# Kernel tuning notes

Measured on AMD Instinct MI355X. Metric: run time of the kernel, lower is better.

## Reference

```python
import jax, jax.numpy as jnp
import numpy as np

B, S, H, C = 512, 16, 501, 7


def _uniform(k, shape, scale):
    return jax.random.uniform(k, shape, minval=-scale, maxval=scale, dtype=jnp.float32)


def setup_inputs() -> dict:
    key = jax.random.key(0)
    ks = jax.random.split(key, 20)
    s = 1.0 / np.sqrt(H)        # torch default init bound for Linear(H, .) and GRUCell
    se = 1.0 / np.sqrt(2 * H)   # Linear(2H, 1)
    z = jax.random.normal(ks[0], (B, H), jnp.float32)
    # strictly-lower-triangular 0/1 adjacency (DAG, ancestors have smaller index)
    dep = jax.random.randint(ks[1], (B, S, S), 0, 2).astype(jnp.float32)
    dep_graph = dep * jnp.tril(jnp.ones((S, S), jnp.float32), k=-1)
    node_encoding = jax.nn.one_hot(jax.random.randint(ks[2], (B, S), 0, C), C, dtype=jnp.float32)
    return {
        "z": z,
        "dep_graph": dep_graph,
        "node_encoding": node_encoding,
        "W_lin1": _uniform(ks[3], (H, H), s), "b_lin1": _uniform(ks[4], (H,), s),
        "W_vert": _uniform(ks[5], (C, H), s), "b_vert": _uniform(ks[6], (C,), s),
        "W_edge": _uniform(ks[7], (1, 2 * H), se), "b_edge": _uniform(ks[8], (1,), se),
        "W_gate": _uniform(ks[9], (H, H), s), "b_gate": _uniform(ks[10], (H,), s),
        "W_map": _uniform(ks[11], (H, H), s), "b_map": _uniform(ks[12], (H,), s),
        "W_ih": _uniform(ks[13], (3 * H, C), s), "b_ih": _uniform(ks[14], (3 * H,), s),
        "W_hh": _uniform(ks[15], (3 * H, H), s), "b_hh": _uniform(ks[16], (3 * H,), s),
    }


def _forward(z, dep_graph, node_encoding, W_lin1, b_lin1, W_vert, b_vert, W_edge, b_edge,
             W_gate, b_gate, W_map, b_map, W_ih, b_ih, W_hh, b_hh):
    Bs, Ss, _ = dep_graph.shape
    Hs = W_lin1.shape[0]

    def gru(x, h):  # torch.nn.GRUCell math
        gi = x @ W_ih.T + b_ih
        gh = h @ W_hh.T + b_hh
        i_r, i_z, i_n = jnp.split(gi, 3, axis=-1)
        h_r, h_z, h_n = jnp.split(gh, 3, axis=-1)
        r = jax.nn.sigmoid(i_r + h_r)
        u = jax.nn.sigmoid(i_z + h_z)
        n = jnp.tanh(i_n + r * h_n)
        return (1.0 - u) * n + u * h

    col = jnp.arange(Ss)

    def outer_step(carry, idx):
        graph_state, nhs = carry  # nhs: (B, S, H) node_hidden_state
        logits = jax.nn.softmax(graph_state @ W_vert.T + b_vert, axis=-1)  # add_vertex
        x_idx = jax.lax.dynamic_index_in_dim(node_encoding, idx, axis=1, keepdims=False)  # (B, C)
        row0 = jax.lax.dynamic_index_in_dim(dep_graph, idx, axis=1, keepdims=False)       # (B, S)

        def inner_step(ic, t):  # v_j = idx-1, ..., 0 (masked when v_j < 0)
            hv, nhs_i, row, edges = ic
            v_j = idx - 1 - t
            active = v_j >= 0
            vj = jnp.maximum(v_j, 0)
            hidden_j = jax.lax.dynamic_index_in_dim(nhs_i, vj, axis=1, keepdims=False)  # (B, H)
            p = jax.nn.sigmoid(jnp.concatenate([hv, hidden_j], axis=-1) @ W_edge.T + b_edge)  # (B,1)
            is_edge = (p[:, 0] >= 0.5).astype(z.dtype)  # hard threshold, as in source
            # emulates the in-place `ancestors[:, :v_j] = 0` on the dep_graph row
            row_new = jnp.where(col[None, :] < vj, 0.0, row)
            anc = (nhs_i * row_new[:, :, None]).reshape(-1, Hs)  # (B*S, H)
            h_in = (jax.nn.sigmoid(anc @ W_gate.T + b_gate) * (anc @ W_map.T + b_map)
                    ).reshape(Bs, Ss, Hs).sum(axis=1)  # gated-sum message aggregation
            hv_new = gru(x_idx, h_in)
            nhs_new = jax.lax.dynamic_update_index_in_dim(nhs_i, hv_new, idx, axis=1)
            edges = jnp.where(active, edges.at[:, vj].set(is_edge), edges)
            hv = jnp.where(active, hv_new, hv)
            nhs_i = jnp.where(active, nhs_new, nhs_i)
            row = jnp.where(active, row_new, row)
            return (hv, nhs_i, row, edges), None

        edges0 = jnp.zeros((Bs, Ss), z.dtype)
        (hv, nhs2, _, edges), _ = jax.lax.scan(
            inner_step, (graph_state, nhs, row0, edges0), jnp.arange(Ss - 1))
        # index == 0: no ancestors; hv = GRU(x_0, graph_state) (source leaves hv undefined here)
        hv = jnp.where(idx == 0, gru(x_idx, graph_state), hv)
        nhs3 = jax.lax.dynamic_update_index_in_dim(nhs2, hv, idx, axis=1)
        return (hv, nhs3), (logits, edges)

    graph_state0 = z @ W_lin1.T + b_lin1
    nhs0 = jnp.zeros((Bs, Ss, Hs), z.dtype)
    _, (enc, rows) = jax.lax.scan(outer_step, (graph_state0, nhs0), jnp.arange(Ss))
    gen_dep_graph = jnp.transpose(rows, (1, 0, 2))      # (B, S, S)
    gen_node_encoding = jnp.transpose(enc, (1, 0, 2))   # (B, S, C)
    return gen_dep_graph, gen_node_encoding


def reference(z, dep_graph, node_encoding, W_lin1, b_lin1, W_vert, b_vert, W_edge, b_edge,
              W_gate, b_gate, W_map, b_map, W_ih, b_ih, W_hh, b_hh):
    return _forward(z, dep_graph, node_encoding, W_lin1, b_lin1, W_vert, b_vert, W_edge,
                    b_edge, W_gate, b_gate, W_map, b_map, W_ih, b_ih, W_hh, b_hh)
```

## Files before the change

kernel.cpp:

```cpp
#include <hip/hip_runtime.h>
#include <math.h>

#define BB 512
#define SS 16
#define HH 501
#define CC 7
#define CH 128
#define PBK (4*BB)
#define OFF_ENC (BB*SS*SS)

#define BUFSZ (132*PBK)
#define O_BUFIN 0
#define O_BUFH  BUFSZ
#define O_ALIST (2*BUFSZ)
#define O_ELIST (O_ALIST + SS*BB)
#define O_CLS   (O_ELIST + SS*BB)

__device__ __forceinline__ float4 ld4(const float* p) { return *(const float4*)p; }
__device__ __forceinline__ float sigm(float x) { return 1.f / (1.f + expf(-x)); }

__device__ __forceinline__ int PACK(int k, int b) {
    return (k >> 2) * PBK + b * 4 + (k & 3);
}

__global__ __launch_bounds__(256) void k_prep(
    const float* __restrict__ z, const float* __restrict__ xenc,
    float* __restrict__ bufH, int* __restrict__ cls, float* __restrict__ out)
{
    const int b = blockIdx.x, tid = threadIdx.x;
    if (b < 256) {
        __shared__ float t[32][33];
        const int bt = b >> 4, kt = b & 15;
        const int b0 = bt * 32, k0 = kt * 32;
        const int tx = tid & 31, ty = tid >> 5;
#pragma unroll
        for (int i = 0; i < 4; ++i) {
            int row = ty + i * 8;
            t[row][tx] = (k0 + tx < HH) ? z[(b0 + row) * HH + k0 + tx] : 0.f;
        }
        __syncthreads();
#pragma unroll
        for (int i = 0; i < 4; ++i) {
            int row = ty + i * 8;
            int k = k0 + row;
            float v = (k < HH) ? t[tx][row] : 0.f;
            bufH[PACK(k, b0 + tx)] = v;
        }
    } else if (b < 264) {
        int base = (b - 256) * 1024 + tid * 4;
#pragma unroll
        for (int q = 0; q < 4; ++q) {
            int e = base + q; int s = e >> 9, bb = e & 511;
            const float* xp = xenc + (bb * SS + s) * CC;
            int c = 0;
#pragma unroll
            for (int cc = 0; cc < CC; ++cc) if (xp[cc] > 0.5f) c = cc;
            cls[s * BB + bb] = c;
        }
    } else {
        float4 z4 = make_float4(0.f, 0.f, 0.f, 0.f);
        float4* o4 = (float4*)out;
#pragma unroll
        for (int q = 0; q < 4; ++q)
            o4[(b - 264) * 1024 + q * 256 + tid] = z4;
    }
}

__global__ __launch_bounds__(256) void k_g0(
    const float* __restrict__ act, const float* __restrict__ W,
    const float* __restrict__ blin1, float* __restrict__ dst)
{
    __shared__ float wl[4][520];
    const int tid = threadIdx.x, lane = tid & 63;
    const int wv = __builtin_amdgcn_readfirstlane(tid >> 6);
    const int rg = blockIdx.x >> 2, ch = blockIdx.x & 3;
    const int r = rg * 4 + wv;
#pragma unroll
    for (int j = 0; j < 4; ++j) {
        int rr = rg * 4 + j;
        const float* src = W + (size_t)min(rr, HH - 1) * HH;
        bool ok = rr < HH;
        for (int k = tid; k < 512; k += 256)
            wl[j][k] = (ok && k < HH) ? src[k] : 0.f;
    }
    __syncthreads();
    const int c0 = ch * 128 + lane, c1 = c0 + 64;
    const float* a0 = act + c0 * 4;
    const float* a1 = act + c1 * 4;
    float4 A0[4], A1[4], Wb[2];
#pragma unroll
    for (int q = 0; q < 3; ++q) { A0[q] = ld4(a0 + q * PBK); A1[q] = ld4(a1 + q * PBK); }
    Wb[0] = ld4(&wl[wv][0]);
    float s0 = 0.f, s1 = 0.f;
#pragma unroll 4
    for (int kc = 0; kc < CH; ++kc) {
        int kn = kc + 3;
        A0[kn & 3] = ld4(a0 + (size_t)kn * PBK);
        A1[kn & 3] = ld4(a1 + (size_t)kn * PBK);
        int kw = min(kc + 1, CH - 1);
        Wb[(kc + 1) & 1] = ld4(&wl[wv][kw * 4]);
        float4 w = Wb[kc & 1], x0 = A0[kc & 3], x1 = A1[kc & 3];
        s0 = fmaf(w.x, x0.x, s0); s0 = fmaf(w.y, x0.y, s0);
        s0 = fmaf(w.z, x0.z, s0); s0 = fmaf(w.w, x0.w, s0);
        s1 = fmaf(w.x, x1.x, s1); s1 = fmaf(w.y, x1.y, s1);
        s1 = fmaf(w.z, x1.z, s1); s1 = fmaf(w.w, x1.w, s1);
    }
    if (r < HH) {
        float bv = blin1[r];
        dst[PACK(r, c0)] = s0 + bv;
        dst[PACK(r, c1)] = s1 + bv;
    }
}

__global__ __launch_bounds__(256) void k_gru(
    const float* __restrict__ act, const float* __restrict__ Whh,
    const int* __restrict__ cls,
    const float* __restrict__ bhh, const float* __restrict__ Wih,
    const float* __restrict__ bih, int idx, float* __restrict__ dst)
{
    __shared__ float wl[12][520];
    const int tid = threadIdx.x, lane = tid & 63;
    const int wv = __builtin_amdgcn_readfirstlane(tid >> 6);
    const int rg = blockIdx.x >> 2, ch = blockIdx.x & 3;
    const int r = rg * 4 + wv;
#pragma unroll
    for (int j = 0; j < 12; ++j) {
        int g = j >> 2, rl = j & 3, rr = rg * 4 + rl;
        const float* src = Whh + (size_t)(g * HH + min(rr, HH - 1)) * HH;
        bool ok = rr < HH;
        for (int k = tid; k < 512; k += 256)
            wl[j][k] = (ok && k < HH) ? src[k] : 0.f;
    }
    const int c0 = ch * 128 + lane, c1 = c0 + 64;
    const int cc0 = cls[idx * BB + c0], cc1 = cls[idx * BB + c1];
    const float hp0 = act[PACK(min(r, HH - 1), c0)];
    const float hp1 = act[PACK(min(r, HH - 1), c1)];
    __syncthreads();
    const float* a0 = act + c0 * 4;
    const float* a1 = act + c1 * 4;
    float4 A0[4], A1[4], Wb[2][3];
#pragma unroll
    for (int q = 0; q < 3; ++q) { A0[q] = ld4(a0 + q * PBK); A1[q] = ld4(a1 + q * PBK); }
#pragma unroll
    for (int g = 0; g < 3; ++g) Wb[0][g] = ld4(&wl[g * 4 + wv][0]);
    float acc[6] = {};
#pragma unroll 4
    for (int kc = 0; kc < CH; ++kc) {
        int kn = kc + 3;
        A0[kn & 3] = ld4(a0 + (size_t)kn * PBK);
        A1[kn & 3] = ld4(a1 + (size_t)kn * PBK);
        int kw = min(kc + 1, CH - 1);
#pragma unroll
        for (int g = 0; g < 3; ++g) Wb[(kc + 1) & 1][g] = ld4(&wl[g * 4 + wv][kw * 4]);
        float4 x0 = A0[kc & 3], x1 = A1[kc & 3];
#pragma unroll
        for (int g = 0; g < 3; ++g) {
            float4 w = Wb[kc & 1][g];
            acc[g*2+0] = fmaf(w.x, x0.x, acc[g*2+0]); acc[g*2+0] = fmaf(w.y, x0.y, acc[g*2+0]);
            acc[g*2+0] = fmaf(w.z, x0.z, acc[g*2+0]); acc[g*2+0] = fmaf(w.w, x0.w, acc[g*2+0]);
            acc[g*2+1] = fmaf(w.x, x1.x, acc[g*2+1]); acc[g*2+1] = fmaf(w.y, x1.y, acc[g*2+1]);
            acc[g*2+1] = fmaf(w.z, x1.z, acc[g*2+1]); acc[g*2+1] = fmaf(w.w, x1.w, acc[g*2+1]);
        }
    }
    if (r < HH) {
        float bi0 = bih[r], bi1 = bih[HH + r], bi2 = bih[2 * HH + r];
        float bh0 = bhh[r], bh1 = bhh[HH + r], bh2 = bhh[2 * HH + r];
        float w0c0 = Wih[(0 * HH + r) * CC + cc0], w1c0 = Wih[(1 * HH + r) * CC + cc0],
              w2c0 = Wih[(2 * HH + r) * CC + cc0];
        float w0c1 = Wih[(0 * HH + r) * CC + cc1], w1c1 = Wih[(1 * HH + r) * CC + cc1],
              w2c1 = Wih[(2 * HH + r) * CC + cc1];
        {
            float rgt = sigm(w0c0 + bi0 + acc[0] + bh0);
            float ugt = sigm(w1c0 + bi1 + acc[2] + bh1);
            float ngt = tanhf(w2c0 + bi2 + rgt * (acc[4] + bh2));
            dst[PACK(r, c0)] = (1.f - ugt) * ngt + ugt * hp0;
        }
        {
            float rgt = sigm(w0c1 + bi0 + acc[1] + bh0);
            float ugt = sigm(w1c1 + bi1 + acc[3] + bh1);
            float ngt = tanhf(w2c1 + bi2 + rgt * (acc[5] + bh2));
            dst[PACK(r, c1)] = (1.f - ugt) * ngt + ugt * hp1;
        }
    }
}

__global__ __launch_bounds__(256) void k_post(
    const float* __restrict__ actH, const float* __restrict__ actIn,
    const float* __restrict__ Wgate, const float* __restrict__ bgate,
    const float* __restrict__ Wmap,  const float* __restrict__ bmap,
    const float* __restrict__ dep,
    const float* __restrict__ Wedge, const float* __restrict__ bedge,
    const float* __restrict__ Wvert, const float* __restrict__ bvert,
    int idx, int ngemm, int dsrc,
    float* __restrict__ dst, float* __restrict__ Alist,
    float* __restrict__ Elist, float* __restrict__ out)
{
    __shared__ float wl[9][520];
    const int tid = threadIdx.x, lane = tid & 63;
    const int wv = __builtin_amdgcn_readfirstlane(tid >> 6);
    if ((int)blockIdx.x < ngemm) {
        const int rg = blockIdx.x >> 2, ch = blockIdx.x & 3;
        const int r = rg * 4 + wv;
#pragma unroll
        for (int j = 0; j < 8; ++j) {
            int t2 = j >> 2, rl = j & 3, rr = rg * 4 + rl;
            const float* src = (t2 ? Wmap : Wgate) + (size_t)min(rr, HH - 1) * HH;
            bool ok = rr < HH;
            for (int k = tid; k < 512; k += 256)
                wl[j][k] = (ok && k < HH) ? src[k] : 0.f;
        }
        const int c0 = ch * 128 + lane, c1 = c0 + 64;
        const float d0 = dep[c0 * (SS * SS) + (idx + 1) * SS + idx];
        const float d1 = dep[c1 * (SS * SS) + (idx + 1) * SS + idx];
        __syncthreads();
        const float* a0 = actH + c0 * 4;
        const float* a1 = actH + c1 * 4;
        float4 A0[4], A1[4], Wb[2][2];
#pragma unroll
        for (int q = 0; q < 3; ++q) { A0[q] = ld4(a0 + q * PBK); A1[q] = ld4(a1 + q * PBK); }
#pragma unroll
        for (int t2 = 0; t2 < 2; ++t2) Wb[0][t2] = ld4(&wl[t2 * 4 + wv][0]);
        float acc[4] = {};
#pragma unroll 4
        for (int kc = 0; kc < CH; ++kc) {
            int kn = kc + 3;
            A0[kn & 3] = ld4(a0 + (size_t)kn * PBK);
            A1[kn & 3] = ld4(a1 + (size_t)kn * PBK);
            int kw = min(kc + 1, CH - 1);
#pragma unroll
            for (int t2 = 0; t2 < 2; ++t2) Wb[(kc + 1) & 1][t2] = ld4(&wl[t2 * 4 + wv][kw * 4]);
            float4 x0 = A0[kc & 3], x1 = A1[kc & 3];
#pragma unroll
            for (int t2 = 0; t2 < 2; ++t2) {
                float4 w = Wb[kc & 1][t2];
                acc[t2*2+0] = fmaf(w.x, x0.x, acc[t2*2+0]); acc[t2*2+0] = fmaf(w.y, x0.y, acc[t2*2+0]);
                acc[t2*2+0] = fmaf(w.z, x0.z, acc[t2*2+0]); acc[t2*2+0] = fmaf(w.w, x0.w, acc[t2*2+0]);
                acc[t2*2+1] = fmaf(w.x, x1.x, acc[t2*2+1]); acc[t2*2+1] = fmaf(w.y, x1.y, acc[t2*2+1]);
                acc[t2*2+1] = fmaf(w.z, x1.z, acc[t2*2+1]); acc[t2*2+1] = fmaf(w.w, x1.w, acc[t2*2+1]);
            }
        }
        if (r < HH) {
            float bgv = bgate[r], bmv = bmap[r];
            float c0v = sigm(bgv) * bmv;
            float f0 = sigm(acc[0] + bgv) * (acc[2] + bmv);
            float f1 = sigm(acc[1] + bgv) * (acc[3] + bmv);
            dst[PACK(r, c0)] = (d0 != 0.f) ? (f0 + 15.f * c0v) : (16.f * c0v);
            dst[PACK(r, c1)] = (d1 != 0.f) ? (f1 + 15.f * c0v) : (16.f * c0v);
        }
    } else {
#pragma unroll
        for (int j = 0; j < 9; ++j) {
            const float* src = (j < 2) ? (Wedge + j * HH) : (Wvert + (j - 2) * HH);
            for (int k = tid; k < 512; k += 256)
                wl[j][k] = (k < HH) ? src[k] : 0.f;
        }
        __syncthreads();
        const int db = ((int)blockIdx.x - ngemm) * 256 + tid;
        const float* hp = (dsrc ? actH : actIn) + db * 4;
        float4 Ab[4];
#pragma unroll
        for (int q = 0; q < 3; ++q) Ab[q] = ld4(hp + q * PBK);
        float p[9];
#pragma unroll
        for (int j = 0; j < 9; ++j) p[j] = 0.f;
#pragma unroll 4
        for (int kc = 0; kc < CH; ++kc) {
            int kn = kc + 3;
            Ab[kn & 3] = ld4(hp + (size_t)kn * PBK);
            float4 x = Ab[kc & 3];
#pragma unroll
            for (int j = 0; j < 9; ++j) {
                float4 w = ld4(&wl[j][kc * 4]);
                p[j] = fmaf(w.x, x.x, p[j]); p[j] = fmaf(w.y, x.y, p[j]);
                p[j] = fmaf(w.z, x.z, p[j]); p[j] = fmaf(w.w, x.w, p[j]);
            }
        }
        if (idx >= 0) { Alist[idx * BB + db] = p[0]; Elist[idx * BB + db] = p[1]; }
        if (idx <= SS - 2) {
            float lv[CC]; float mx = -1e30f;
#pragma unroll
            for (int c = 0; c < CC; ++c) { lv[c] = p[2 + c] + bvert[c]; mx = fmaxf(mx, lv[c]); }
            float sum = 0.f; float ev[CC];
#pragma unroll
            for (int c = 0; c < CC; ++c) { ev[c] = expf(lv[c] - mx); sum += ev[c]; }
            float inv = 1.f / sum;
#pragma unroll
            for (int c = 0; c < CC; ++c)
                out[OFF_ENC + (db * SS + (idx + 1)) * CC + c] = ev[c] * inv;
        }
        if (idx >= 1) {
            float be = bedge[0];
            float aprev = Alist[(idx - 1) * BB + db], eprev = Elist[(idx - 1) * BB + db];
            out[db * SS * SS + idx * SS + (idx - 1)] =
                (aprev + eprev + be >= 0.f) ? 1.f : 0.f;
            for (int vj = 0; vj <= idx - 2; ++vj)
                out[db * SS * SS + idx * SS + vj] =
                    (p[0] + Elist[vj * BB + db] + be >= 0.f) ? 1.f : 0.f;
        }
    }
}

extern "C" void kernel_launch(void* const* d_in, const int* in_sizes, int n_in,
                              void* d_out, int out_size, void* d_ws, size_t ws_size,
                              hipStream_t stream)
{
    const float* z     = (const float*)d_in[0];
    const float* dep   = (const float*)d_in[1];
    const float* xenc  = (const float*)d_in[2];
    const float* Wlin1 = (const float*)d_in[3];
    const float* blin1 = (const float*)d_in[4];
    const float* Wvert = (const float*)d_in[5];
    const float* bvert = (const float*)d_in[6];
    const float* Wedge = (const float*)d_in[7];
    const float* bedge = (const float*)d_in[8];
    const float* Wgate = (const float*)d_in[9];
    const float* bgate = (const float*)d_in[10];
    const float* Wmap  = (const float*)d_in[11];
    const float* bmap  = (const float*)d_in[12];
    const float* Wih   = (const float*)d_in[13];
    const float* bih   = (const float*)d_in[14];
    const float* Whh   = (const float*)d_in[15];
    const float* bhh   = (const float*)d_in[16];
    float* out = (float*)d_out;

    float* ws    = (float*)d_ws;
    float* bufIn = ws + O_BUFIN;
    float* bufH  = ws + O_BUFH;
    float* Alist = ws + O_ALIST;
    float* Elist = ws + O_ELIST;
    int*   cls   = (int*)(ws + O_CLS);

    k_prep<<<296, 256, 0, stream>>>(z, xenc, bufH, cls, out);
    k_g0<<<504, 256, 0, stream>>>(bufH, Wlin1, blin1, bufIn);
    k_post<<<2, 256, 0, stream>>>(bufH, bufIn, Wgate, bgate, Wmap, bmap, dep,
                                  Wedge, bedge, Wvert, bvert, -1, 0, 0,
                                  bufIn, Alist, Elist, out);
    for (int idx = 0; idx < SS; ++idx) {
        k_gru<<<504, 256, 0, stream>>>(bufIn, Whh, cls, bhh, Wih, bih, idx, bufH);
        int ng = (idx < SS - 1) ? 504 : 0;
        k_post<<<ng + 2, 256, 0, stream>>>(bufH, bufIn, Wgate, bgate, Wmap, bmap,
                                           dep, Wedge, bedge, Wvert, bvert,
                                           idx, ng, 1,
                                           bufIn, Alist, Elist, out);
    }
}
```

Baseline: 1.319 ms.

## Move GRU and post GEMMs to bf16x3 split-precision MFMA with prepacked weights

Replaces the FP32 FMA GEMV-style kernels with MFMA 16x16x32 bf16 matrix-core kernels. FP32 accuracy is approximated by splitting each operand into hi and lo bf16 parts and issuing three MFMAs per product. Weights are converted once into a fragment-ready bf16 layout. Activations are also written in transposed bf16 hi/lo form alongside the packed fp32 buffer. This targets the FP32 ALU cost of the recurrent per-step GEMMs, at the price of extra conversion work, more workspace, and a small precision risk.

```diff
diff --git a/kernel.cpp b/kernel.cpp
--- a/kernel.cpp
+++ b/kernel.cpp
@@ -5,7 +5,7 @@
 #define SS 16
 #define HH 501
 #define CC 7
-#define CH 128
+#define KP 512
 #define PBK (4*BB)
 #define OFF_ENC (BB*SS*SS)
 
@@ -15,288 +15,376 @@
 #define O_ALIST (2*BUFSZ)
 #define O_ELIST (O_ALIST + SS*BB)
 #define O_CLS   (O_ELIST + SS*BB)
-
-__device__ __forceinline__ float4 ld4(const float* p) { return *(const float4*)p; }
+#define O_ZT    (O_CLS + SS*BB)
+#define O_INT   (O_ZT  + 262144)
+#define O_HT    (O_INT + 262144)
+#define O_WLIN  (O_HT  + 262144)
+#define O_WPOST (O_WLIN + 262144)
+#define O_WHH   (O_WPOST + 524288)
+#define O_WDOT  (O_WHH + 786432)
+
+typedef __attribute__((ext_vector_type(8))) short bfrag;
+typedef __attribute__((ext_vector_type(4))) float ffrag;
+
 __device__ __forceinline__ float sigm(float x) { return 1.f / (1.f + expf(-x)); }
 
-__device__ __forceinline__ int PACK(int k, int b) {
-    return (k >> 2) * PBK + b * 4 + (k & 3);
-}
-
-__global__ __launch_bounds__(256) void k_prep(
+__device__ __forceinline__ unsigned short f2bf(float x) {
+    unsigned u = __float_as_uint(x);
+    u = u + 0x7fffu + ((u >> 16) & 1u);
+    return (unsigned short)(u >> 16);
+}
+__device__ __forceinline__ float bf2f(unsigned short h) {
+    return __uint_as_float(((unsigned)h) << 16);
+}
+
+__global__ __launch_bounds__(256) void k_wprep(
+    const float* __restrict__ Wlin1, const float* __restrict__ Wgate,
+    const float* __restrict__ Wmap,  const float* __restrict__ Whh,
+    const float* __restrict__ Wedge, const float* __restrict__ Wvert,
+    unsigned short* __restrict__ wlin, unsigned short* __restrict__ wpost,
+    unsigned short* __restrict__ whhf, unsigned short* __restrict__ wdot)
+{
+    const int id = blockIdx.x * 256 + threadIdx.x;
+    const int slot = id >> 10, rem = id & 1023, s = rem >> 6, lane = rem & 63;
+    const int rloc = lane & 15;
+    const int k0 = s * 32 + ((lane >> 4) << 3);
+    const float* src; unsigned short* dst; int dslot; bool valid;
+    if (slot < 32) {
+        int row = slot * 16 + rloc; valid = row < HH;
+        src = Wlin1 + (size_t)(valid ? row : 0) * HH; dst = wlin; dslot = slot;
+    } else if (slot < 96) {
+        int p = slot - 32, g = p >> 5, mt = p & 31;
+        int row = mt * 16 + rloc; valid = row < HH;
+        src = (g ? Wmap : Wgate) + (size_t)(valid ? row : 0) * HH; dst = wpost; dslot = p;
+    } else if (slot < 192) {
+        int p = slot - 96, g = p >> 5, mt = p & 31;
+        int row = mt * 16 + rloc; valid = row < HH;
+        src = Whh + (size_t)(g * HH + (valid ? row : 0)) * HH; dst = whhf; dslot = p;
+    } else {
+        int row = rloc; dst = wdot; dslot = 0;
+        if (row < 2)      { src = Wedge + (size_t)row * HH; valid = true; }
+        else if (row < 9) { src = Wvert + (size_t)(row - 2) * HH; valid = true; }
+        else              { src = Wedge; valid = false; }
+    }
+    unsigned h[8], l[8];
+#pragma unroll
+    for (int j = 0; j < 8; ++j) {
+        int k = k0 + j;
+        float w = (valid && k < HH) ? src[k] : 0.f;
+        unsigned short hb = f2bf(w);
+        h[j] = hb; l[j] = f2bf(w - bf2f(hb));
+    }
+    size_t base = ((size_t)dslot * 32 + s * 2) * 512 + lane * 8;
+    uint4 uh, ul;
+    uh.x = h[0] | (h[1] << 16); uh.y = h[2] | (h[3] << 16);
+    uh.z = h[4] | (h[5] << 16); uh.w = h[6] | (h[7] << 16);
+    ul.x = l[0] | (l[1] << 16); ul.y = l[2] | (l[3] << 16);
+    ul.z = l[4] | (l[5] << 16); ul.w = l[6] | (l[7] << 16);
+    *(uint4*)&dst[base] = uh;
+    *(uint4*)&dst[base + 512] = ul;
+}
+
+__global__ __launch_bounds__(256) void k_prep2(
     const float* __restrict__ z, const float* __restrict__ xenc,
-    float* __restrict__ bufH, int* __restrict__ cls, float* __restrict__ out)
+    unsigned short* __restrict__ zTh, unsigned short* __restrict__ zTl,
+    int* __restrict__ cls, float* __restrict__ out)
 {
     const int b = blockIdx.x, tid = threadIdx.x;
-    if (b < 256) {
-        __shared__ float t[32][33];
-        const int bt = b >> 4, kt = b & 15;
-        const int b0 = bt * 32, k0 = kt * 32;
-        const int tx = tid & 31, ty = tid >> 5;
-#pragma unroll
-        for (int i = 0; i < 4; ++i) {
-            int row = ty + i * 8;
-            t[row][tx] = (k0 + tx < HH) ? z[(b0 + row) * HH + k0 + tx] : 0.f;
-        }
-        __syncthreads();
-#pragma unroll
-        for (int i = 0; i < 4; ++i) {
-            int row = ty + i * 8;
-            int k = k0 + row;
-            float v = (k < HH) ? t[tx][row] : 0.f;
-            bufH[PACK(k, b0 + tx)] = v;
-        }
-    } else if (b < 264) {
-        int base = (b - 256) * 1024 + tid * 4;
+    if (b < 128) {
+        const int id = b * 256 + tid;
+        const int bb = id >> 6, kc = id & 63, k0 = kc * 8;
+        unsigned h[8], l[8];
+#pragma unroll
+        for (int j = 0; j < 8; ++j) {
+            int k = k0 + j;
+            float w = (k < HH) ? z[(size_t)bb * HH + k] : 0.f;
+            unsigned short hb = f2bf(w);
+            h[j] = hb; l[j] = f2bf(w - bf2f(hb));
+        }
+        uint4 uh, ul;
+        uh.x = h[0] | (h[1] << 16); uh.y = h[2] | (h[3] << 16);
+        uh.z = h[4] | (h[5] << 16); uh.w = h[6] | (h[7] << 16);
+        ul.x = l[0] | (l[1] << 16); ul.y = l[2] | (l[3] << 16);
+        ul.z = l[4] | (l[5] << 16); ul.w = l[6] | (l[7] << 16);
+        *(uint4*)&zTh[(size_t)bb * 512 + k0] = uh;
+        *(uint4*)&zTl[(size_t)bb * 512 + k0] = ul;
+    } else if (b < 136) {
+        int base = (b - 128) * 1024 + tid * 4;
 #pragma unroll
         for (int q = 0; q < 4; ++q) {
-            int e = base + q; int s = e >> 9, bb = e & 511;
-            const float* xp = xenc + (bb * SS + s) * CC;
-            int c = 0;
-#pragma unroll
-            for (int cc = 0; cc < CC; ++cc) if (xp[cc] > 0.5f) c = cc;
-            cls[s * BB + bb] = c;
+            int e = base + q, sI = e >> 9, bb = e & 511;
+            const float* xp = xenc + ((size_t)bb * SS + sI) * CC;
+            int cv = 0;
+#pragma unroll
+            for (int cc = 0; cc < CC; ++cc) if (xp[cc] > 0.5f) cv = cc;
+            cls[sI * BB + bb] = cv;
         }
     } else {
         float4 z4 = make_float4(0.f, 0.f, 0.f, 0.f);
         float4* o4 = (float4*)out;
 #pragma unroll
         for (int q = 0; q < 4; ++q)
-            o4[(b - 264) * 1024 + q * 256 + tid] = z4;
-    }
-}
-
-__global__ __launch_bounds__(256) void k_g0(
-    const float* __restrict__ act, const float* __restrict__ W,
-    const float* __restrict__ blin1, float* __restrict__ dst)
-{
-    __shared__ float wl[4][520];
-    const int tid = threadIdx.x, lane = tid & 63;
-    const int wv = __builtin_amdgcn_readfirstlane(tid >> 6);
-    const int rg = blockIdx.x >> 2, ch = blockIdx.x & 3;
-    const int r = rg * 4 + wv;
-#pragma unroll
-    for (int j = 0; j < 4; ++j) {
-        int rr = rg * 4 + j;
-        const float* src = W + (size_t)min(rr, HH - 1) * HH;
-        bool ok = rr < HH;
-        for (int k = tid; k < 512; k += 256)
-            wl[j][k] = (ok && k < HH) ? src[k] : 0.f;
-    }
+            o4[(b - 136) * 1024 + q * 256 + tid] = z4;
+    }
+}
+
+template<int G>
+__device__ __forceinline__ void gemm_core(
+    const unsigned short* __restrict__ wf,
+    const unsigned short* __restrict__ bTh, const unsigned short* __restrict__ bTl,
+    int mt0, int c0, int lane, ffrag* acc)
+{
+    const char* wp  = (const char*)wf  + (size_t)lane * 16;
+    const char* bph = (const char*)bTh + (size_t)(c0 + (lane & 15)) * 1024 + ((lane >> 4) * 16);
+    const char* bpl = (const char*)bTl + (size_t)(c0 + (lane & 15)) * 1024 + ((lane >> 4) * 16);
+#pragma unroll
+    for (int s = 0; s < 16; ++s) {
+        bfrag bh[2], bl[2];
+#pragma unroll
+        for (int n = 0; n < 2; ++n) {
+            bh[n] = *(const bfrag*)(bph + n * 16384 + s * 64);
+            bl[n] = *(const bfrag*)(bpl + n * 16384 + s * 64);
+        }
+#pragma unroll
+        for (int g = 0; g < G; ++g) {
+#pragma unroll
+            for (int m = 0; m < 2; ++m) {
+                const char* ap = wp + (size_t)((g * 32 + mt0 + m) * 32 + s * 2) * 1024;
+                bfrag ah = *(const bfrag*)ap;
+                bfrag al = *(const bfrag*)(ap + 1024);
+#pragma unroll
+                for (int n = 0; n < 2; ++n) {
+                    ffrag* A = acc + (g * 2 + m) * 2 + n;
+                    *A = __builtin_amdgcn_mfma_f32_16x16x32_bf16(ah, bh[n], *A, 0, 0, 0);
+                    *A = __builtin_amdgcn_mfma_f32_16x16x32_bf16(ah, bl[n], *A, 0, 0, 0);
+                    *A = __builtin_amdgcn_mfma_f32_16x16x32_bf16(al, bh[n], *A, 0, 0, 0);
+                }
+            }
+        }
+    }
+}
+
+__device__ __forceinline__ void store_pack(float* __restrict__ dst, int rbase, int c, const float* v) {
+    float* p = dst + (size_t)(rbase >> 2) * PBK + c * 4;
+    if (rbase + 3 < HH) {
+        *(float4*)p = make_float4(v[0], v[1], v[2], v[3]);
+    } else {
+#pragma unroll
+        for (int i = 0; i < 4; ++i) if (rbase + i < HH) p[i] = v[i];
+    }
+}
+
+__device__ __forceinline__ void store_T(unsigned short* __restrict__ Th, unsigned short* __restrict__ Tl,
+                                        int c, int rbase, const float* v) {
+    unsigned h[4], l[4];
+#pragma unroll
+    for (int i = 0; i < 4; ++i) {
+        unsigned short hb = f2bf(v[i]);
+        h[i] = hb; l[i] = f2bf(v[i] - bf2f(hb));
+    }
+    uint2 uh, ul;
+    uh.x = h[0] | (h[1] << 16); uh.y = h[2] | (h[3] << 16);
+    ul.x = l[0] | (l[1] << 16); ul.y = l[2] | (l[3] << 16);
+    *(uint2*)&Th[(size_t)c * 512 + rbase] = uh;
+    *(uint2*)&Tl[(size_t)c * 512 + rbase] = ul;
+}
+
+__global__ __launch_bounds__(128, 1) void k_g0m(
+    const unsigned short* __restrict__ zTh, const unsigned short* __restrict__ zTl,
+    const unsigned short* __restrict__ wlin, const float* __restrict__ blin1,
+    float* __restrict__ dstPack, unsigned short* __restrict__ Th, unsigned short* __restrict__ Tl)
+{
+    const int tid = threadIdx.x, lane = tid & 63, wv = tid >> 6;
+    const int rb = blockIdx.x >> 3, cbb = blockIdx.x & 7;
+    const int mt0 = rb * 2, c0 = (cbb * 2 + wv) * 32;
+    const ffrag fz = {0.f, 0.f, 0.f, 0.f};
+    ffrag acc[4];
+#pragma unroll
+    for (int i = 0; i < 4; ++i) acc[i] = fz;
+    gemm_core<1>(wlin, zTh, zTl, mt0, c0, lane, acc);
+#pragma unroll
+    for (int m = 0; m < 2; ++m) {
+        const int rbase = (mt0 + m) * 16 + ((lane >> 4) << 2);
+#pragma unroll
+        for (int n = 0; n < 2; ++n) {
+            const int c = c0 + n * 16 + (lane & 15);
+            float v[4];
+#pragma unroll
+            for (int r = 0; r < 4; ++r) {
+                int rr = rbase + r;
+                v[r] = (rr < HH) ? acc[m * 2 + n][r] + blin1[rr] : 0.f;
+            }
+            store_pack(dstPack, rbase, c, v);
+            store_T(Th, Tl, c, rbase, v);
+        }
+    }
+}
+
+__global__ __launch_bounds__(128, 1) void k_grum(
+    const unsigned short* __restrict__ inTh, const unsigned short* __restrict__ inTl,
+    const unsigned short* __restrict__ whhf, const float* __restrict__ hinPack,
+    const int* __restrict__ cls, const float* __restrict__ Wih,
+    const float* __restrict__ bih, const float* __restrict__ bhh,
+    int idx, unsigned short* __restrict__ Th, unsigned short* __restrict__ Tl)
+{
+    const int tid = threadIdx.x, lane = tid & 63, wv = tid >> 6;
+    const int rb = blockIdx.x >> 3, cbb = blockIdx.x & 7;
+    const int mt0 = rb * 2, c0 = (cbb * 2 + wv) * 32;
+    const ffrag fz = {0.f, 0.f, 0.f, 0.f};
+    ffrag acc[12];
+#pragma unroll
+    for (int i = 0; i < 12; ++i) acc[i] = fz;
+    gemm_core<3>(whhf, inTh, inTl, mt0, c0, lane, acc);
+#pragma unroll
+    for (int m = 0; m < 2; ++m) {
+        const int rbase = (mt0 + m) * 16 + ((lane >> 4) << 2);
+#pragma unroll
+        for (int n = 0; n < 2; ++n) {
+            const int c = c0 + n * 16 + (lane & 15);
+            const int cc = cls[idx * BB + c];
+            float hp[4];
+            { float4 t = *(const float4*)&hinPack[(size_t)(rbase >> 2) * PBK + c * 4];
+              hp[0] = t.x; hp[1] = t.y; hp[2] = t.z; hp[3] = t.w; }
+            float v[4];
+#pragma unroll
+            for (int r = 0; r < 4; ++r) {
+                int rr = rbase + r;
+                if (rr < HH) {
+                    float ar  = acc[(0 * 2 + m) * 2 + n][r];
+                    float az  = acc[(1 * 2 + m) * 2 + n][r];
+                    float an2 = acc[(2 * 2 + m) * 2 + n][r];
+                    float rgt = sigm(Wih[(size_t)rr * CC + cc] + bih[rr] + ar + bhh[rr]);
+                    float ugt = sigm(Wih[(size_t)(HH + rr) * CC + cc] + bih[HH + rr] + az + bhh[HH + rr]);
+                    float ngt = tanhf(Wih[(size_t)(2 * HH + rr) * CC + cc] + bih[2 * HH + rr]
+                                      + rgt * (an2 + bhh[2 * HH + rr]));
+                    v[r] = (1.f - ugt) * ngt + ugt * hp[r];
+                } else v[r] = 0.f;
+            }
+            store_T(Th, Tl, c, rbase, v);
+        }
+    }
+}
+
+__device__ __forceinline__ void dots_body(
+    int blk8, int tid, int lane, int wv,
+    const unsigned short* __restrict__ Th, const unsigned short* __restrict__ Tl,
+    const unsigned short* __restrict__ wdot, const float* __restrict__ bvert,
+    const float* __restrict__ bedge, float* __restrict__ Alist, float* __restrict__ Elist,
+    int idx, float* __restrict__ out, float (*dls)[65])
+{
+    const int c0 = (blk8 * 2 + wv) * 32;
+    const ffrag fz = {0.f, 0.f, 0.f, 0.f};
+    ffrag acc[2]; acc[0] = fz; acc[1] = fz;
+    const char* wp  = (const char*)wdot + (size_t)lane * 16;
+    const char* bph = (const char*)Th + (size_t)(c0 + (lane & 15)) * 1024 + ((lane >> 4) * 16);
+    const char* bpl = (const char*)Tl + (size_t)(c0 + (lane & 15)) * 1024 + ((lane >> 4) * 16);
+#pragma unroll
+    for (int s = 0; s < 16; ++s) {
+        bfrag ah = *(const bfrag*)(wp + (size_t)(s * 2) * 1024);
+        bfrag al = *(const bfrag*)(wp + (size_t)(s * 2 + 1) * 1024);
+#pragma unroll
+        for (int n = 0; n < 2; ++n) {
+            bfrag bh = *(const bfrag*)(bph + n * 16384 + s * 64);
+            bfrag bl = *(const bfrag*)(bpl + n * 16384 + s * 64);
+            acc[n] = __builtin_amdgcn_mfma_f32_16x16x32_bf16(ah, bh, acc[n], 0, 0, 0);
+            acc[n] = __builtin_amdgcn_mfma_f32_16x16x32_bf16(ah, bl, acc[n], 0, 0, 0);
+            acc[n] = __builtin_amdgcn_mfma_f32_16x16x32_bf16(al, bh, acc[n], 0, 0, 0);
+        }
+    }
+#pragma unroll
+    for (int n = 0; n < 2; ++n)
+#pragma unroll
+        for (int r = 0; r < 4; ++r)
+            dls[((lane >> 4) << 2) + r][wv * 32 + n * 16 + (lane & 15)] = acc[n][r];
     __syncthreads();
-    const int c0 = ch * 128 + lane, c1 = c0 + 64;
-    const float* a0 = act + c0 * 4;
-    const float* a1 = act + c1 * 4;
-    float4 A0[4], A1[4], Wb[2];
-#pragma unroll
-    for (int q = 0; q < 3; ++q) { A0[q] = ld4(a0 + q * PBK); A1[q] = ld4(a1 + q * PBK); }
-    Wb[0] = ld4(&wl[wv][0]);
-    float s0 = 0.f, s1 = 0.f;
-#pragma unroll 4
-    for (int kc = 0; kc < CH; ++kc) {
-        int kn = kc + 3;
-        A0[kn & 3] = ld4(a0 + (size_t)kn * PBK);
-        A1[kn & 3] = ld4(a1 + (size_t)kn * PBK);
-        int kw = min(kc + 1, CH - 1);
-        Wb[(kc + 1) & 1] = ld4(&wl[wv][kw * 4]);
-        float4 w = Wb[kc & 1], x0 = A0[kc & 3], x1 = A1[kc & 3];
-        s0 = fmaf(w.x, x0.x, s0); s0 = fmaf(w.y, x0.y, s0);
-        s0 = fmaf(w.z, x0.z, s0); s0 = fmaf(w.w, x0.w, s0);
-        s1 = fmaf(w.x, x1.x, s1); s1 = fmaf(w.y, x1.y, s1);
-        s1 = fmaf(w.z, x1.z, s1); s1 = fmaf(w.w, x1.w, s1);
-    }
-    if (r < HH) {
-        float bv = blin1[r];
-        dst[PACK(r, c0)] = s0 + bv;
-        dst[PACK(r, c1)] = s1 + bv;
-    }
-}
-
-__global__ __launch_bounds__(256) void k_gru(
-    const float* __restrict__ act, const float* __restrict__ Whh,
-    const int* __restrict__ cls,
-    const float* __restrict__ bhh, const float* __restrict__ Wih,
-    const float* __restrict__ bih, int idx, float* __restrict__ dst)
-{
-    __shared__ float wl[12][520];
-    const int tid = threadIdx.x, lane = tid & 63;
-    const int wv = __builtin_amdgcn_readfirstlane(tid >> 6);
-    const int rg = blockIdx.x >> 2, ch = blockIdx.x & 3;
-    const int r = rg * 4 + wv;
-#pragma unroll
-    for (int j = 0; j < 12; ++j) {
-        int g = j >> 2, rl = j & 3, rr = rg * 4 + rl;
-        const float* src = Whh + (size_t)(g * HH + min(rr, HH - 1)) * HH;
-        bool ok = rr < HH;
-        for (int k = tid; k < 512; k += 256)
-            wl[j][k] = (ok && k < HH) ? src[k] : 0.f;
-    }
-    const int c0 = ch * 128 + lane, c1 = c0 + 64;
-    const int cc0 = cls[idx * BB + c0], cc1 = cls[idx * BB + c1];
-    const float hp0 = act[PACK(min(r, HH - 1), c0)];
-    const float hp1 = act[PACK(min(r, HH - 1), c1)];
-    __syncthreads();
-    const float* a0 = act + c0 * 4;
-    const float* a1 = act + c1 * 4;
-    float4 A0[4], A1[4], Wb[2][3];
-#pragma unroll
-    for (int q = 0; q < 3; ++q) { A0[q] = ld4(a0 + q * PBK); A1[q] = ld4(a1 + q * PBK); }
-#pragma unroll
-    for (int g = 0; g < 3; ++g) Wb[0][g] = ld4(&wl[g * 4 + wv][0]);
-    float acc[6] = {};
-#pragma unroll 4
-    for (int kc = 0; kc < CH; ++kc) {
-        int kn = kc + 3;
-        A0[kn & 3] = ld4(a0 + (size_t)kn * PBK);
-        A1[kn & 3] = ld4(a1 + (size_t)kn * PBK);
-        int kw = min(kc + 1, CH - 1);
-#pragma unroll
-        for (int g = 0; g < 3; ++g) Wb[(kc + 1) & 1][g] = ld4(&wl[g * 4 + wv][kw * 4]);
-        float4 x0 = A0[kc & 3], x1 = A1[kc & 3];
-#pragma unroll
-        for (int g = 0; g < 3; ++g) {
-            float4 w = Wb[kc & 1][g];
-            acc[g*2+0] = fmaf(w.x, x0.x, acc[g*2+0]); acc[g*2+0] = fmaf(w.y, x0.y, acc[g*2+0]);
-            acc[g*2+0] = fmaf(w.z, x0.z, acc[g*2+0]); acc[g*2+0] = fmaf(w.w, x0.w, acc[g*2+0]);
-            acc[g*2+1] = fmaf(w.x, x1.x, acc[g*2+1]); acc[g*2+1] = fmaf(w.y, x1.y, acc[g*2+1]);
-            acc[g*2+1] = fmaf(w.z, x1.z, acc[g*2+1]); acc[g*2+1] = fmaf(w.w, x1.w, acc[g*2+1]);
-        }
-    }
-    if (r < HH) {
-        float bi0 = bih[r], bi1 = bih[HH + r], bi2 = bih[2 * HH + r];
-        float bh0 = bhh[r], bh1 = bhh[HH + r], bh2 = bhh[2 * HH + r];
-        float w0c0 = Wih[(0 * HH + r) * CC + cc0], w1c0 = Wih[(1 * HH + r) * CC + cc0],
-              w2c0 = Wih[(2 * HH + r) * CC + cc0];
-        float w0c1 = Wih[(0 * HH + r) * CC + cc1], w1c1 = Wih[(1 * HH + r) * CC + cc1],
-              w2c1 = Wih[(2 * HH + r) * CC + cc1];
-        {
-            float rgt = sigm(w0c0 + bi0 + acc[0] + bh0);
-            float ugt = sigm(w1c0 + bi1 + acc[2] + bh1);
-            float ngt = tanhf(w2c0 + bi2 + rgt * (acc[4] + bh2));
-            dst[PACK(r, c0)] = (1.f - ugt) * ngt + ugt * hp0;
-        }
-        {
-            float rgt = sigm(w0c1 + bi0 + acc[1] + bh0);
-            float ugt = sigm(w1c1 + bi1 + acc[3] + bh1);
-            float ngt = tanhf(w2c1 + bi2 + rgt * (acc[5] + bh2));
-            dst[PACK(r, c1)] = (1.f - ugt) * ngt + ugt * hp1;
-        }
-    }
-}
-
-__global__ __launch_bounds__(256) void k_post(
-    const float* __restrict__ actH, const float* __restrict__ actIn,
-    const float* __restrict__ Wgate, const float* __restrict__ bgate,
-    const float* __restrict__ Wmap,  const float* __restrict__ bmap,
-    const float* __restrict__ dep,
-    const float* __restrict__ Wedge, const float* __restrict__ bedge,
-    const float* __restrict__ Wvert, const float* __restrict__ bvert,
-    int idx, int ngemm, int dsrc,
-    float* __restrict__ dst, float* __restrict__ Alist,
-    float* __restrict__ Elist, float* __restrict__ out)
-{
-    __shared__ float wl[9][520];
-    const int tid = threadIdx.x, lane = tid & 63;
-    const int wv = __builtin_amdgcn_readfirstlane(tid >> 6);
-    if ((int)blockIdx.x < ngemm) {
-        const int rg = blockIdx.x >> 2, ch = blockIdx.x & 3;
-        const int r = rg * 4 + wv;
-#pragma unroll
-        for (int j = 0; j < 8; ++j) {
-            int t2 = j >> 2, rl = j & 3, rr = rg * 4 + rl;
-            const float* src = (t2 ? Wmap : Wgate) + (size_t)min(rr, HH - 1) * HH;
-            bool ok = rr < HH;
-            for (int k = tid; k < 512; k += 256)
-                wl[j][k] = (ok && k < HH) ? src[k] : 0.f;
-        }
-        const int c0 = ch * 128 + lane, c1 = c0 + 64;
-        const float d0 = dep[c0 * (SS * SS) + (idx + 1) * SS + idx];
-        const float d1 = dep[c1 * (SS * SS) + (idx + 1) * SS + idx];
-        __syncthreads();
-        const float* a0 = actH + c0 * 4;
-        const float* a1 = actH + c1 * 4;
-        float4 A0[4], A1[4], Wb[2][2];
-#pragma unroll
-        for (int q = 0; q < 3; ++q) { A0[q] = ld4(a0 + q * PBK); A1[q] = ld4(a1 + q * PBK); }
-#pragma unroll
-        for (int t2 = 0; t2 < 2; ++t2) Wb[0][t2] = ld4(&wl[t2 * 4 + wv][0]);
-        float acc[4] = {};
-#pragma unroll 4
-        for (int kc = 0; kc < CH; ++kc) {
-            int kn = kc + 3;
-            A0[kn & 3] = ld4(a0 + (size_t)kn * PBK);
-            A1[kn & 3] = ld4(a1 + (size_t)kn * PBK);
-            int kw = min(kc + 1, CH - 1);
-#pragma unroll
-            for (int t2 = 0; t2 < 2; ++t2) Wb[(kc + 1) & 1][t2] = ld4(&wl[t2 * 4 + wv][kw * 4]);
-            float4 x0 = A0[kc & 3], x1 = A1[kc & 3];
-#pragma unroll
-            for (int t2 = 0; t2 < 2; ++t2) {
-                float4 w = Wb[kc & 1][t2];
-                acc[t2*2+0] = fmaf(w.x, x0.x, acc[t2*2+0]); acc[t2*2+0] = fmaf(w.y, x0.y, acc[t2*2+0]);
-                acc[t2*2+0] = fmaf(w.z, x0.z, acc[t2*2+0]); acc[t2*2+0] = fmaf(w.w, x0.w, acc[t2*2+0]);
-                acc[t2*2+1] = fmaf(w.x, x1.x, acc[t2*2+1]); acc[t2*2+1] = fmaf(w.y, x1.y, acc[t2*2+1]);
-                acc[t2*2+1] = fmaf(w.z, x1.z, acc[t2*2+1]); acc[t2*2+1] = fmaf(w.w, x1.w, acc[t2*2+1]);
-            }
-        }
-        if (r < HH) {
-            float bgv = bgate[r], bmv = bmap[r];
-            float c0v = sigm(bgv) * bmv;
-            float f0 = sigm(acc[0] + bgv) * (acc[2] + bmv);
-            float f1 = sigm(acc[1] + bgv) * (acc[3] + bmv);
-            dst[PACK(r, c0)] = (d0 != 0.f) ? (f0 + 15.f * c0v) : (16.f * c0v);
-            dst[PACK(r, c1)] = (d1 != 0.f) ? (f1 + 15.f * c0v) : (16.f * c0v);
-        }
-    } else {
-#pragma unroll
-        for (int j = 0; j < 9; ++j) {
-            const float* src = (j < 2) ? (Wedge + j * HH) : (Wvert + (j - 2) * HH);
-            for (int k = tid; k < 512; k += 256)
-                wl[j][k] = (k < HH) ? src[k] : 0.f;
-        }
-        __syncthreads();
-        const int db = ((int)blockIdx.x - ngemm) * 256 + tid;
-        const float* hp = (dsrc ? actH : actIn) + db * 4;
-        float4 Ab[4];
-#pragma unroll
-        for (int q = 0; q < 3; ++q) Ab[q] = ld4(hp + q * PBK);
-        float p[9];
-#pragma unroll
-        for (int j = 0; j < 9; ++j) p[j] = 0.f;
-#pragma unroll 4
-        for (int kc = 0; kc < CH; ++kc) {
-            int kn = kc + 3;
-            Ab[kn & 3] = ld4(hp + (size_t)kn * PBK);
-            float4 x = Ab[kc & 3];
-#pragma unroll
-            for (int j = 0; j < 9; ++j) {
-                float4 w = ld4(&wl[j][kc * 4]);
-                p[j] = fmaf(w.x, x.x, p[j]); p[j] = fmaf(w.y, x.y, p[j]);
-                p[j] = fmaf(w.z, x.z, p[j]); p[j] = fmaf(w.w, x.w, p[j]);
-            }
-        }
-        if (idx >= 0) { Alist[idx * BB + db] = p[0]; Elist[idx * BB + db] = p[1]; }
+    if (tid < 64) {
+        const int b = blk8 * 64 + tid;
+        float v[9];
+#pragma unroll
+        for (int j = 0; j < 9; ++j) v[j] = dls[j][tid];
+        if (idx >= 0) { Alist[idx * BB + b] = v[0]; Elist[idx * BB + b] = v[1]; }
         if (idx <= SS - 2) {
-            float lv[CC]; float mx = -1e30f;
-#pragma unroll
-            for (int c = 0; c < CC; ++c) { lv[c] = p[2 + c] + bvert[c]; mx = fmaxf(mx, lv[c]); }
-            float sum = 0.f; float ev[CC];
+            float lv[CC], mx = -1e30f;
+#pragma unroll
+            for (int c = 0; c < CC; ++c) { lv[c] = v[2 + c] + bvert[c]; mx = fmaxf(mx, lv[c]); }
+            float sum = 0.f, ev[CC];
 #pragma unroll
             for (int c = 0; c < CC; ++c) { ev[c] = expf(lv[c] - mx); sum += ev[c]; }
             float inv = 1.f / sum;
 #pragma unroll
             for (int c = 0; c < CC; ++c)
-                out[OFF_ENC + (db * SS + (idx + 1)) * CC + c] = ev[c] * inv;
+                out[OFF_ENC + ((size_t)b * SS + (idx + 1)) * CC + c] = ev[c] * inv;
         }
         if (idx >= 1) {
             float be = bedge[0];
-            float aprev = Alist[(idx - 1) * BB + db], eprev = Elist[(idx - 1) * BB + db];
-            out[db * SS * SS + idx * SS + (idx - 1)] =
+            float aprev = Alist[(idx - 1) * BB + b], eprev = Elist[(idx - 1) * BB + b];
+            out[(size_t)b * SS * SS + idx * SS + (idx - 1)] =
                 (aprev + eprev + be >= 0.f) ? 1.f : 0.f;
             for (int vj = 0; vj <= idx - 2; ++vj)
-                out[db * SS * SS + idx * SS + vj] =
-                    (p[0] + Elist[vj * BB + db] + be >= 0.f) ? 1.f : 0.f;
-        }
+                out[(size_t)b * SS * SS + idx * SS + vj] =
+                    (v[0] + Elist[vj * BB + b] + be >= 0.f) ? 1.f : 0.f;
+        }
+    }
+}
+
+__global__ __launch_bounds__(128, 1) void k_dotsm(
+    const unsigned short* __restrict__ Th, const unsigned short* __restrict__ Tl,
+    const unsigned short* __restrict__ wdot, const float* __restrict__ bvert,
+    const float* __restrict__ bedge, float* __restrict__ Alist, float* __restrict__ Elist,
+    int idx, float* __restrict__ out)
+{
+    __shared__ float dls[16][65];
+    dots_body(blockIdx.x, threadIdx.x, threadIdx.x & 63, threadIdx.x >> 6,
+              Th, Tl, wdot, bvert, bedge, Alist, Elist, idx, out, dls);
+}
+
+__global__ __launch_bounds__(128, 1) void k_postm(
+    const unsigned short* __restrict__ hTh, const unsigned short* __restrict__ hTl,
+    const unsigned short* __restrict__ wpostf,
+    const float* __restrict__ bgate, const float* __restrict__ bmap,
+    const float* __restrict__ dep,
+    const unsigned short* __restrict__ wdot, const float* __restrict__ bvert,
+    const float* __restrict__ bedge, float* __restrict__ Alist, float* __restrict__ Elist,
+    int idx, float* __restrict__ dstPack,
+    unsigned short* __restrict__ Th, unsigned short* __restrict__ Tl,
+    float* __restrict__ out)
+{
+    __shared__ float dls[16][65];
+    const int tid = threadIdx.x, lane = tid & 63, wv = tid >> 6;
+    if ((int)blockIdx.x < 128) {
+        const int rb = blockIdx.x >> 3, cbb = blockIdx.x & 7;
+        const int mt0 = rb * 2, c0 = (cbb * 2 + wv) * 32;
+        const ffrag fz = {0.f, 0.f, 0.f, 0.f};
+        ffrag acc[8];
+#pragma unroll
+        for (int i = 0; i < 8; ++i) acc[i] = fz;
+        gemm_core<2>(wpostf, hTh, hTl, mt0, c0, lane, acc);
+#pragma unroll
+        for (int m = 0; m < 2; ++m) {
+            const int rbase = (mt0 + m) * 16 + ((lane >> 4) << 2);
+#pragma unroll
+            for (int n = 0; n < 2; ++n) {
+                const int c = c0 + n * 16 + (lane & 15);
+                const float d = dep[(size_t)c * (SS * SS) + (idx + 1) * SS + idx];
+                float v[4];
+#pragma unroll
+                for (int r = 0; r < 4; ++r) {
+                    int rr = rbase + r;
+                    if (rr < HH) {
+                        float bg = bgate[rr], bm = bmap[rr];
+                        float cv = sigm(bg) * bm;
+                        float f = sigm(acc[(0 * 2 + m) * 2 + n][r] + bg)
+                                * (acc[(1 * 2 + m) * 2 + n][r] + bm);
+                        v[r] = (d != 0.f) ? (f + 15.f * cv) : (16.f * cv);
+                    } else v[r] = 0.f;
+                }
+                store_pack(dstPack, rbase, c, v);
+                store_T(Th, Tl, c, rbase, v);
+            }
+        }
+    } else {
+        dots_body((int)blockIdx.x - 128, tid, lane, wv,
+                  hTh, hTl, wdot, bvert, bedge, Alist, Elist, idx, out, dls);
     }
 }
 
@@ -325,22 +413,34 @@
 
     float* ws    = (float*)d_ws;
     float* bufIn = ws + O_BUFIN;
-    float* bufH  = ws + O_BUFH;
     float* Alist = ws + O_ALIST;
     float* Elist = ws + O_ELIST;
     int*   cls   = (int*)(ws + O_CLS);
-
-    k_prep<<<296, 256, 0, stream>>>(z, xenc, bufH, cls, out);
-    k_g0<<<504, 256, 0, stream>>>(bufH, Wlin1, blin1, bufIn);
-    k_post<<<2, 256, 0, stream>>>(bufH, bufIn, Wgate, bgate, Wmap, bmap, dep,
-                                  Wedge, bedge, Wvert, bvert, -1, 0, 0,
-                                  bufIn, Alist, Elist, out);
+    unsigned short* zTh  = (unsigned short*)(ws + O_ZT);
+    unsigned short* zTl  = zTh + 262144;
+    unsigned short* inTh = (unsigned short*)(ws + O_INT);
+    unsigned short* inTl = inTh + 262144;
+    unsigned short* hTh  = (unsigned short*)(ws + O_HT);
+    unsigned short* hTl  = hTh + 262144;
+    unsigned short* wlin  = (unsigned short*)(ws + O_WLIN);
+    unsigned short* wpost = (unsigned short*)(ws + O_WPOST);
+    unsigned short* whhf  = (unsigned short*)(ws + O_WHH);
+    unsigned short* wdot  = (unsigned short*)(ws + O_WDOT);
+
+    k_wprep<<<772, 256, 0, stream>>>(Wlin1, Wgate, Wmap, Whh, Wedge, Wvert,
+                                     wlin, wpost, whhf, wdot);
+    k_prep2<<<168, 256, 0, stream>>>(z, xenc, zTh, zTl, cls, out);
+    k_g0m<<<128, 128, 0, stream>>>(zTh, zTl, wlin, blin1, bufIn, inTh, inTl);
+    k_dotsm<<<8, 128, 0, stream>>>(inTh, inTl, wdot, bvert, bedge, Alist, Elist, -1, out);
     for (int idx = 0; idx < SS; ++idx) {
-        k_gru<<<504, 256, 0, stream>>>(bufIn, Whh, cls, bhh, Wih, bih, idx, bufH);
-        int ng = (idx < SS - 1) ? 504 : 0;
-        k_post<<<ng + 2, 256, 0, stream>>>(bufH, bufIn, Wgate, bgate, Wmap, bmap,
-                                           dep, Wedge, bedge, Wvert, bvert,
-                                           idx, ng, 1,
-                                           bufIn, Alist, Elist, out);
-    }
-}
+        k_grum<<<128, 128, 0, stream>>>(inTh, inTl, whhf, bufIn, cls, Wih, bih, bhh,
+                                        idx, hTh, hTl);
+        if (idx < SS - 1)
+            k_postm<<<136, 128, 0, stream>>>(hTh, hTl, wpost, bgate, bmap, dep,
+                                             wdot, bvert, bedge, Alist, Elist,
+                                             idx, bufIn, inTh, inTl, out);
+        else
+            k_dotsm<<<8, 128, 0, stream>>>(hTh, hTl, wdot, bvert, bedge, Alist, Elist,
+                                           idx, out);
+    }
+}
```

After: 1.109 ms. 1.19x faster.
